# Performance work log

Hardware: AMD Instinct MI355X
Metric: run time of the kernel (lower is better)

The kernel has to match this reference:

```python
import jax, jax.numpy as jnp
import numpy as np
from jax import lax

IMG_H = IMG_W = 800.0
PRE_NMS = 2000      # rpn_pre_nms_top_n (test)
POST_NMS = 1000     # rpn_post_nms_top_n (test)
IOU_THR = 0.7       # rpn nms_thresh
MIN_SIZE = 1e-3     # filter_proposals min_size
SCORE_THR = 0.0     # rpn score_thresh
BBOX_CLIP = float(np.log(1000.0 / 16.0))  # torchvision BoxCoder bbox_xform_clip


def setup_inputs() -> dict:
    key = jax.random.key(0)
    k1, k2, k3, k4 = jax.random.split(key, 4)
    N, A = 8, 1_000_000
    objectness = jax.random.normal(k1, (N, A), jnp.float32)
    deltas = jax.random.normal(k2, (N, A, 4), jnp.float32) * 0.5
    # realistic anchors: random centers inside the image, sizes in [16, 256]
    cxy = jax.random.uniform(k3, (A, 2), jnp.float32) * jnp.array([IMG_W, IMG_H], jnp.float32)
    wh = 16.0 + jax.random.uniform(k4, (A, 2), jnp.float32) * 240.0
    anchors = jnp.concatenate([cxy - 0.5 * wh, cxy + 0.5 * wh], axis=-1)
    return {"objectness": objectness, "deltas": deltas, "anchors": anchors}


def decode_boxes(deltas, anchors):
    # torchvision BoxCoder.decode_single with weights (1,1,1,1)
    wa = anchors[:, 2] - anchors[:, 0]          # [A]
    ha = anchors[:, 3] - anchors[:, 1]
    cxa = anchors[:, 0] + 0.5 * wa
    cya = anchors[:, 1] + 0.5 * ha
    dx, dy = deltas[..., 0], deltas[..., 1]      # [N, A]
    dw = jnp.minimum(deltas[..., 2], BBOX_CLIP)
    dh = jnp.minimum(deltas[..., 3], BBOX_CLIP)
    pcx = dx * wa + cxa
    pcy = dy * ha + cya
    pw = jnp.exp(dw) * wa
    ph = jnp.exp(dh) * ha
    return jnp.stack([pcx - 0.5 * pw, pcy - 0.5 * ph,
                      pcx + 0.5 * pw, pcy + 0.5 * ph], axis=-1)  # [N, A, 4]


def nms_keep(boxes, valid):
    # greedy NMS on score-sorted boxes [K,4]; returns boolean keep mask [K]
    K = boxes.shape[0]
    areas = (boxes[:, 2] - boxes[:, 0]) * (boxes[:, 3] - boxes[:, 1])
    idxs = jnp.arange(K)

    def body(i, keep):
        xx1 = jnp.maximum(boxes[i, 0], boxes[:, 0])
        yy1 = jnp.maximum(boxes[i, 1], boxes[:, 1])
        xx2 = jnp.minimum(boxes[i, 2], boxes[:, 2])
        yy2 = jnp.minimum(boxes[i, 3], boxes[:, 3])
        inter = jnp.maximum(xx2 - xx1, 0.0) * jnp.maximum(yy2 - yy1, 0.0)
        iou = inter / (areas[i] + areas - inter + 1e-12)
        sup = (iou > IOU_THR) & (idxs > i) & keep[i]
        return keep & ~sup

    return lax.fori_loop(0, K, body, valid)


def filter_one(obj, boxes):
    # per-image filter_proposals: top-k -> sigmoid -> clip -> small-box removal -> NMS -> top post_nms
    top_logits, idx = lax.top_k(obj, PRE_NMS)        # sorted desc; sigmoid is monotone
    b = boxes[idx]                                    # [K, 4]
    scores = jax.nn.sigmoid(top_logits)
    x1 = jnp.clip(b[:, 0], 0.0, IMG_W)
    y1 = jnp.clip(b[:, 1], 0.0, IMG_H)
    x2 = jnp.clip(b[:, 2], 0.0, IMG_W)
    y2 = jnp.clip(b[:, 3], 0.0, IMG_H)
    bc = jnp.stack([x1, y1, x2, y2], axis=-1)
    valid = ((x2 - x1) >= MIN_SIZE) & ((y2 - y1) >= MIN_SIZE) & (scores > SCORE_THR)
    keep = nms_keep(lax.stop_gradient(bc), valid)     # selection is non-differentiable
    masked = jnp.where(keep, scores, -jnp.inf)
    _, fidx = lax.top_k(lax.stop_gradient(masked), POST_NMS)
    out_boxes = bc[fidx]                              # [POST_NMS, 4]
    out_scores = jnp.where(keep[fidx], scores[fidx], 0.0)
    return out_boxes, out_scores


def reference(objectness, deltas, anchors):
    proposals = decode_boxes(deltas, anchors)                 # [N, A, 4]
    boxes, scores = jax.vmap(filter_one)(objectness, proposals)
    return jnp.concatenate([boxes, scores[:, :, None]], axis=-1)  # [N, POST_NMS, 5]
```

## Files before the change

kernel.cpp:

```cpp
#include <hip/hip_runtime.h>
#include <cstdint>

#define NIMG 8
#define PRE 2000
#define POST 1000
#define NCH 64
#define CH_CAP 256
#define CAND_TOT (NCH*CH_CAP)
#define NSORT 4
#define SEG 2048
#define CAND_MAX (NSORT*SEG)
#define NPB 64
#define PB_CAP 1024
#define PAIR_CAP 12288
#define JT 256
#define IMGW 800.0f
#define BBOX_CLIP_F 4.135166556742356f
#define STATIC_KMIN 0xC0200000u

#define OFF_BCNT  0
#define OFF_BPCNT (OFF_BCNT + NIMG*NCH*4)
#define OFF_CAND  (OFF_BPCNT + NIMG*NPB*4)
#define OFF_SRT   (OFF_CAND + NIMG*CAND_TOT*8)
#define OFF_BOX   (OFF_SRT + NIMG*CAND_MAX*8)
#define OFF_SCORE (OFF_BOX + NIMG*PRE*16)
#define OFF_VALID (OFF_SCORE + NIMG*PRE*4)
#define OFF_PAIRS (OFF_VALID + NIMG*PRE*4)

__device__ __forceinline__ unsigned int fkey(float f) {
    unsigned int b = __float_as_uint(f);
    return (b & 0x80000000u) ? ~b : (b | 0x80000000u);
}
__device__ __forceinline__ float inv_fkey(unsigned int k) {
    unsigned int b = (k & 0x80000000u) ? (k ^ 0x80000000u) : ~k;
    return __uint_as_float(b);
}

__global__ void k_compact(const float* __restrict__ obj,
                          unsigned long long* __restrict__ cand,
                          unsigned int* __restrict__ bcnt, int A) {
    __shared__ unsigned long long loc[CH_CAP];
    __shared__ unsigned int lcnt;
    const int img = blockIdx.y;
    const int b = blockIdx.x;
    const int t = threadIdx.x;
    if (t == 0) lcnt = 0u;
    __syncthreads();
    const float4* p4 = (const float4*)(obj + (size_t)img * A);
    const int nvec = A >> 2;
    for (int i = b * 256 + t; i < nvec; i += NCH * 256) {
        float4 v = p4[i];
        unsigned int k0 = fkey(v.x), k1 = fkey(v.y), k2 = fkey(v.z), k3 = fkey(v.w);
        unsigned int base = (unsigned int)(i << 2);
        if (k0 >= STATIC_KMIN) { unsigned int p = atomicAdd(&lcnt, 1u); if (p < CH_CAP) loc[p] = ((unsigned long long)k0 << 32) | (0xFFFFFFFFu - base); }
        if (k1 >= STATIC_KMIN) { unsigned int p = atomicAdd(&lcnt, 1u); if (p < CH_CAP) loc[p] = ((unsigned long long)k1 << 32) | (0xFFFFFFFFu - (base + 1u)); }
        if (k2 >= STATIC_KMIN) { unsigned int p = atomicAdd(&lcnt, 1u); if (p < CH_CAP) loc[p] = ((unsigned long long)k2 << 32) | (0xFFFFFFFFu - (base + 2u)); }
        if (k3 >= STATIC_KMIN) { unsigned int p = atomicAdd(&lcnt, 1u); if (p < CH_CAP) loc[p] = ((unsigned long long)k3 << 32) | (0xFFFFFFFFu - (base + 3u)); }
    }
    if (b == 0) {
        const float* p = obj + (size_t)img * A;
        for (int i = (nvec << 2) + t; i < A; i += 256) {
            unsigned int k = fkey(p[i]);
            if (k >= STATIC_KMIN) { unsigned int q = atomicAdd(&lcnt, 1u); if (q < CH_CAP) loc[q] = ((unsigned long long)k << 32) | (0xFFFFFFFFu - (unsigned int)i); }
        }
    }
    __syncthreads();
    if (t == 0) bcnt[img * NCH + b] = lcnt;
    unsigned int n = min(lcnt, (unsigned int)CH_CAP);
    unsigned long long* dst = cand + (size_t)img * CAND_TOT + (size_t)b * CH_CAP;
    for (unsigned int i = t; i < n; i += 256) dst[i] = loc[i];
}

__global__ __launch_bounds__(1024) void k_fallback(const float* __restrict__ obj,
                                                   unsigned long long* __restrict__ cand,
                                                   unsigned int* __restrict__ bcnt, int A) {
    __shared__ unsigned int h[4096];
    __shared__ unsigned int cnts[NCH];
    __shared__ int need_s;
    __shared__ unsigned int kth_s, c2;
    const int img = blockIdx.x;
    const int t = threadIdx.x;
    if (t < NCH) cnts[t] = bcnt[img * NCH + t];
    __syncthreads();
    if (t == 0) {
        unsigned int tot = 0; int bad = 0;
        for (int c = 0; c < NCH; ++c) { unsigned int r = cnts[c]; if (r > CH_CAP) bad = 1; tot += min(r, (unsigned int)CH_CAP); }
        for (int g = 0; g < NSORT; ++g) {
            unsigned int s = 0;
            for (int c = 0; c < NCH / NSORT; ++c) s += min(cnts[g * (NCH / NSORT) + c], (unsigned int)CH_CAP);
            if (s > SEG) bad = 1;
        }
        if (tot < PRE) bad = 1;
        need_s = bad;
    }
    __syncthreads();
    if (!need_s) return;
    for (int i = t; i < 4096; i += 1024) h[i] = 0u;
    __syncthreads();
    const float* p = obj + (size_t)img * A;
    for (int i = t; i < A; i += 1024) atomicAdd(&h[fkey(p[i]) >> 20], 1u);
    __syncthreads();
    if (t == 0) {
        unsigned int run = 0, kb = 0;
        for (int b = 4095; b >= 0; --b) { run += h[b]; if (run >= (unsigned int)PRE) { kb = (unsigned int)b; break; } }
        kth_s = kb << 20; c2 = 0u;
    }
    __syncthreads();
    for (int i = t; i < A; i += 1024) {
        unsigned int k = fkey(p[i]);
        if (k >= kth_s) {
            unsigned int q = atomicAdd(&c2, 1u);
            if (q < CAND_MAX)
                cand[(size_t)img * CAND_TOT + (size_t)(q & (NCH - 1)) * CH_CAP + (q >> 6)] =
                    ((unsigned long long)k << 32) | (0xFFFFFFFFu - (unsigned int)i);
        }
    }
    __syncthreads();
    unsigned int tot = min(c2, (unsigned int)CAND_MAX);
    if (t < NCH) bcnt[img * NCH + t] = (tot + (NCH - 1) - t) >> 6;
}

__global__ __launch_bounds__(1024) void k_sort(const unsigned long long* __restrict__ cand,
                                               const unsigned int* __restrict__ bcnt,
                                               unsigned long long* __restrict__ srt) {
    __shared__ unsigned long long sb[SEG];
    __shared__ unsigned int pref[17];
    const int img = blockIdx.y;
    const int s = blockIdx.x;
    const int t = threadIdx.x;
    if (t == 0) {
        unsigned int o = 0; pref[0] = 0;
        for (int c = 0; c < 16; ++c) {
            unsigned int n = min(bcnt[img * NCH + s * 16 + c], (unsigned int)CH_CAP);
            o += n; if (o > (unsigned int)SEG) o = SEG;
            pref[c + 1] = o;
        }
    }
    for (int i = t; i < SEG; i += 1024) sb[i] = 0ull;
    __syncthreads();
    for (int c = 0; c < 16; ++c) {
        unsigned int b0 = pref[c], n = pref[c + 1] - pref[c];
        const unsigned long long* src = cand + (size_t)img * CAND_TOT + (size_t)(s * 16 + c) * CH_CAP;
        for (unsigned int i = t; i < n; i += 1024) sb[b0 + i] = src[i];
    }
    __syncthreads();
    for (int k = 2; k <= SEG; k <<= 1) {
        for (int j = k >> 1; j > 0; j >>= 1) {
            for (int i = t; i < SEG; i += 1024) {
                int l = i ^ j;
                if (l > i) {
                    unsigned long long a = sb[i], b = sb[l];
                    bool sw = ((i & k) == 0) ? (a < b) : (a > b);
                    if (sw) { sb[i] = b; sb[l] = a; }
                }
            }
            __syncthreads();
        }
    }
    unsigned long long* dst = srt + (size_t)img * CAND_MAX + (size_t)s * SEG;
    for (int i = t; i < SEG; i += 1024) dst[i] = sb[i];
}

__global__ __launch_bounds__(1024) void k_merge_decode(
    const float* __restrict__ deltas, const float* __restrict__ anchors,
    const unsigned long long* __restrict__ srt,
    float* __restrict__ boxes, float* __restrict__ scores, unsigned int* __restrict__ valid, int A) {
    __shared__ unsigned long long sb[CAND_MAX];
    const int img = blockIdx.y;
    const int myseg = blockIdx.x;
    const int t = threadIdx.x;
    const unsigned long long* c = srt + (size_t)img * CAND_MAX;
    for (int i = t; i < CAND_MAX; i += 1024) sb[i] = c[i];
    __syncthreads();
    for (int e2 = t; e2 < SEG; e2 += 1024) {
        const int e = (myseg << 11) + e2;
        unsigned long long v = sb[e];
        if (v == 0ull) continue;
        int rank = e2;
#pragma unroll
        for (int s = 0; s < 4; ++s) {
            if (s == myseg) continue;
            int lo = 0, hi = SEG;
            const unsigned long long* seg = sb + (s << 11);
            while (lo < hi) {
                int mid = (lo + hi) >> 1;
                if (seg[mid] > v) lo = mid + 1; else hi = mid;
            }
            rank += lo;
        }
        if (rank >= PRE) continue;
        unsigned int idx = 0xFFFFFFFFu - (unsigned int)(v & 0xFFFFFFFFull);
        float logit = inv_fkey((unsigned int)(v >> 32));
        float4 d = ((const float4*)deltas)[(size_t)img * A + idx];
        float4 a = ((const float4*)anchors)[idx];
        float wa = a.z - a.x, ha = a.w - a.y;
        float cxa = a.x + 0.5f * wa, cya = a.y + 0.5f * ha;
        float dw = fminf(d.z, BBOX_CLIP_F), dh = fminf(d.w, BBOX_CLIP_F);
        float pcx = d.x * wa + cxa, pcy = d.y * ha + cya;
        float pw = expf(dw) * wa, ph = expf(dh) * ha;
        float x1 = fminf(fmaxf(pcx - 0.5f * pw, 0.0f), IMGW);
        float y1 = fminf(fmaxf(pcy - 0.5f * ph, 0.0f), IMGW);
        float x2 = fminf(fmaxf(pcx + 0.5f * pw, 0.0f), IMGW);
        float y2 = fminf(fmaxf(pcy + 0.5f * ph, 0.0f), IMGW);
        float sc = 1.0f / (1.0f + expf(-logit));
        unsigned int vd = (((x2 - x1) >= 1e-3f) && ((y2 - y1) >= 1e-3f) && (sc > 0.0f)) ? 1u : 0u;
        ((float4*)boxes)[(size_t)img * PRE + rank] = make_float4(x1, y1, x2, y2);
        scores[img * PRE + rank] = sc;
        valid[img * PRE + rank] = vd;
    }
}

__global__ void k_pairs(const float* __restrict__ boxes, unsigned int* __restrict__ pairs,
                        unsigned int* __restrict__ bpcnt) {
#pragma clang fp contract(off)
    const int img = blockIdx.y;
    const int bid = blockIdx.x;
    const int it = bid >> 3;
    const int jc = bid & 7;
    const int t = threadIdx.x;
    if (jc < it) { if (t == 0) bpcnt[img * NPB + bid] = 0u; return; }
    __shared__ float4 jb[JT];
    __shared__ float jar[JT];
    __shared__ unsigned int lp[PB_CAP];
    __shared__ unsigned int lcnt;
    if (t == 0) lcnt = 0u;
    const float4* B = (const float4*)(boxes + (size_t)img * PRE * 4);
    const int j0 = jc * JT;
    const int jn = min(JT, PRE - j0);
    if (t < jn) {
        float4 b = B[j0 + t];
        jb[t] = b;
        jar[t] = (b.z - b.x) * (b.w - b.y);
    }
    const int i = it * JT + t;
    const bool row_ok = (i < PRE);
    float x1 = 0, y1 = 0, x2 = 0, y2 = 0, ai = 0;
    if (row_ok) {
        float4 b = B[i];
        x1 = b.x; y1 = b.y; x2 = b.z; y2 = b.w;
        ai = (b.z - b.x) * (b.w - b.y);
    }
    __syncthreads();
    if (row_ok) {
#pragma unroll 4
        for (int jj = 0; jj < jn; ++jj) {
            float4 bj = jb[jj];
            float aj = jar[jj];
            float xx1 = fmaxf(x1, bj.x);
            float yy1 = fmaxf(y1, bj.y);
            float xx2 = fminf(x2, bj.z);
            float yy2 = fminf(y2, bj.w);
            float iw = fmaxf(xx2 - xx1, 0.0f);
            float ih = fmaxf(yy2 - yy1, 0.0f);
            float inter = iw * ih;
            float iou = inter / (ai + aj - inter + 1e-12f);
            int j = j0 + jj;
            if (iou > 0.7f && j > i) {
                unsigned int p = atomicAdd(&lcnt, 1u);
                if (p < PB_CAP) lp[p] = ((unsigned int)i << 11) | (unsigned int)j;
            }
        }
    }
    __syncthreads();
    unsigned int n = min(lcnt, (unsigned int)PB_CAP);
    if (t == 0) bpcnt[img * NPB + bid] = n;
    unsigned int* dst = pairs + ((size_t)img * NPB + bid) * PB_CAP;
    for (unsigned int q = t; q < n; q += blockDim.x) dst[q] = lp[q];
}

__global__ __launch_bounds__(1024) void k_final(
    const float* __restrict__ boxes, const float* __restrict__ scores, const unsigned int* __restrict__ valid,
    const unsigned int* __restrict__ pairs, const unsigned int* __restrict__ bpcnt, float* __restrict__ out) {
    __shared__ unsigned int pb[PAIR_CAP];
    __shared__ unsigned int bp[NPB];
    __shared__ unsigned int ofs[NPB + 1];
    __shared__ unsigned char vld[2048];
    __shared__ unsigned char alive[2048];
    __shared__ unsigned char kill[2048];
    __shared__ unsigned int incl[2048];
    __shared__ int changed;
    const int img = blockIdx.x;
    const int t = threadIdx.x;
    if (t < NPB) bp[t] = min(bpcnt[img * NPB + t], (unsigned int)PB_CAP);
    __syncthreads();
    if (t == 0) {
        unsigned int o = 0; ofs[0] = 0;
        for (int c = 0; c < NPB; ++c) { o += bp[c]; if (o > (unsigned int)PAIR_CAP) o = PAIR_CAP; ofs[c + 1] = o; }
    }
    for (int i = t; i < 2048; i += 1024) {
        unsigned char v = (i < PRE) ? (unsigned char)valid[img * PRE + i] : 0;
        vld[i] = v;
        alive[i] = v;
    }
    __syncthreads();
    for (int c = 0; c < NPB; ++c) {
        unsigned int b0 = ofs[c], n = ofs[c + 1] - ofs[c];
        const unsigned int* src = pairs + ((size_t)img * NPB + c) * PB_CAP;
        for (unsigned int i = t; i < n; i += 1024) pb[b0 + i] = src[i];
    }
    const int np = (int)ofs[NPB];
    __syncthreads();
    for (int iter = 0; iter < 2048; ++iter) {
        if (t == 0) changed = 0;
        for (int i = t; i < 2048; i += 1024) kill[i] = 0;
        __syncthreads();
        for (int e = t; e < np; e += 1024) {
            unsigned int u = pb[e];
            unsigned int i = u >> 11, j = u & 2047u;
            if (alive[i]) kill[j] = 1;
        }
        __syncthreads();
        for (int i = t; i < 2048; i += 1024) {
            unsigned char na = (vld[i] && !kill[i]) ? 1 : 0;
            if (na != alive[i]) { alive[i] = na; changed = 1; }
        }
        __syncthreads();
        bool done = (changed == 0);
        __syncthreads();
        if (done) break;
    }
    const int i0 = t, i1 = t + 1024;
    incl[i0] = alive[i0]; incl[i1] = alive[i1];
    __syncthreads();
    for (int d = 1; d < 2048; d <<= 1) {
        unsigned int v0 = (i0 >= d) ? incl[i0 - d] : 0u;
        unsigned int v1 = (i1 >= d) ? incl[i1 - d] : 0u;
        __syncthreads();
        incl[i0] += v0; incl[i1] += v1;
        __syncthreads();
    }
    const unsigned int Nk = incl[2047];
    for (int i = t; i < PRE; i += 1024) {
        int slot = -1;
        float sc = 0.0f;
        if (alive[i]) {
            unsigned int r = incl[i] - 1u;
            if (r < (unsigned int)POST) { slot = (int)r; sc = scores[img * PRE + i]; }
        } else if (Nk < (unsigned int)POST) {
            unsigned int rnk = (unsigned int)i - incl[i];
            unsigned int s2 = Nk + rnk;
            if (s2 < (unsigned int)POST) { slot = (int)s2; sc = 0.0f; }
        }
        if (slot >= 0) {
            float4 b = ((const float4*)boxes)[(size_t)img * PRE + i];
            float* o = out + ((size_t)img * POST + slot) * 5;
            o[0] = b.x; o[1] = b.y; o[2] = b.z; o[3] = b.w; o[4] = sc;
        }
    }
}

extern "C" void kernel_launch(void* const* d_in, const int* in_sizes, int n_in,
                              void* d_out, int out_size, void* d_ws, size_t ws_size,
                              hipStream_t stream) {
    const float* obj = (const float*)d_in[0];
    const float* deltas = (const float*)d_in[1];
    const float* anchors = (const float*)d_in[2];
    float* out = (float*)d_out;
    const int A = in_sizes[0] / NIMG;

    char* ws = (char*)d_ws;
    unsigned int* bcnt = (unsigned int*)(ws + OFF_BCNT);
    unsigned int* bpcnt = (unsigned int*)(ws + OFF_BPCNT);
    unsigned long long* cand = (unsigned long long*)(ws + OFF_CAND);
    unsigned long long* srt = (unsigned long long*)(ws + OFF_SRT);
    float* boxes = (float*)(ws + OFF_BOX);
    float* scores = (float*)(ws + OFF_SCORE);
    unsigned int* valid = (unsigned int*)(ws + OFF_VALID);
    unsigned int* pairs = (unsigned int*)(ws + OFF_PAIRS);

    k_compact<<<dim3(NCH, NIMG), dim3(256), 0, stream>>>(obj, cand, bcnt, A);
    k_fallback<<<dim3(NIMG), dim3(1024), 0, stream>>>(obj, cand, bcnt, A);
    k_sort<<<dim3(NSORT, NIMG), dim3(1024), 0, stream>>>(cand, bcnt, srt);
    k_merge_decode<<<dim3(NSORT, NIMG), dim3(1024), 0, stream>>>(deltas, anchors, srt, boxes, scores, valid, A);
    k_pairs<<<dim3(NPB, NIMG), dim3(256), 0, stream>>>(boxes, pairs, bpcnt);
    k_final<<<dim3(NIMG), dim3(1024), 0, stream>>>(boxes, scores, valid, pairs, bpcnt, out);
}
```

Measured before the change: 300.4 us.

## Fuse fallback, segment sort and merge-decode into one kernel with inter-block barrier

Merges the fallback, bitonic segment sort and merge/decode kernels into a single kernel. The four segment blocks of each image synchronise through a global atomic counter spin barrier before ranking across segments. The fallback path now runs inside each block, with every block redoing the histogram and keeping a strided subset of candidates. Compaction also doubles the chunk count and halves the per-chunk capacity. The aim is to cut two kernel launches and their gaps, at the cost of relying on all blocks being co-resident and of redundant fallback work when the fallback fires.

```diff
diff --git a/kernel.cpp b/kernel.cpp
--- a/kernel.cpp
+++ b/kernel.cpp
@@ -4,10 +4,11 @@
 #define NIMG 8
 #define PRE 2000
 #define POST 1000
-#define NCH 64
-#define CH_CAP 256
+#define NCH 128
+#define CH_CAP 128
 #define CAND_TOT (NCH*CH_CAP)
 #define NSORT 4
+#define GPS (NCH/NSORT)
 #define SEG 2048
 #define CAND_MAX (NSORT*SEG)
 #define NPB 64
@@ -19,11 +20,12 @@
 #define STATIC_KMIN 0xC0200000u
 
 #define OFF_BCNT  0
-#define OFF_BPCNT (OFF_BCNT + NIMG*NCH*4)
+#define OFF_DONE  (OFF_BCNT + NIMG*NCH*4)
+#define OFF_BPCNT (OFF_DONE + 1024)
 #define OFF_CAND  (OFF_BPCNT + NIMG*NPB*4)
-#define OFF_SRT   (OFF_CAND + NIMG*CAND_TOT*8)
-#define OFF_BOX   (OFF_SRT + NIMG*CAND_MAX*8)
-#define OFF_SCORE (OFF_BOX + NIMG*PRE*16)
+#define OFF_SRT   (OFF_CAND + (size_t)NIMG*CAND_TOT*8)
+#define OFF_BOX   (OFF_SRT + (size_t)NIMG*CAND_MAX*8)
+#define OFF_SCORE (OFF_BOX + (size_t)NIMG*PRE*16)
 #define OFF_VALID (OFF_SCORE + NIMG*PRE*4)
 #define OFF_PAIRS (OFF_VALID + NIMG*PRE*4)
 
@@ -38,13 +40,17 @@
 
 __global__ void k_compact(const float* __restrict__ obj,
                           unsigned long long* __restrict__ cand,
-                          unsigned int* __restrict__ bcnt, int A) {
+                          unsigned int* __restrict__ bcnt,
+                          unsigned int* __restrict__ done, int A) {
     __shared__ unsigned long long loc[CH_CAP];
     __shared__ unsigned int lcnt;
     const int img = blockIdx.y;
     const int b = blockIdx.x;
     const int t = threadIdx.x;
-    if (t == 0) lcnt = 0u;
+    if (t == 0) {
+        lcnt = 0u;
+        if (b == 0) done[img * 32] = 0u;
+    }
     __syncthreads();
     const float4* p4 = (const float4*)(obj + (size_t)img * A);
     const int nvec = A >> 2;
@@ -71,79 +77,74 @@
     for (unsigned int i = t; i < n; i += 256) dst[i] = loc[i];
 }
 
-__global__ __launch_bounds__(1024) void k_fallback(const float* __restrict__ obj,
-                                                   unsigned long long* __restrict__ cand,
-                                                   unsigned int* __restrict__ bcnt, int A) {
-    __shared__ unsigned int h[4096];
+__global__ __launch_bounds__(1024) void k_sortmerge(
+    const float* __restrict__ obj, const float* __restrict__ deltas, const float* __restrict__ anchors,
+    unsigned long long* __restrict__ cand, const unsigned int* __restrict__ bcnt,
+    unsigned long long* __restrict__ srt, unsigned int* __restrict__ done,
+    float* __restrict__ boxes, float* __restrict__ scores, unsigned int* __restrict__ valid, int A) {
+    __shared__ unsigned long long sb[3 * SEG];
     __shared__ unsigned int cnts[NCH];
-    __shared__ int need_s;
-    __shared__ unsigned int kth_s, c2;
-    const int img = blockIdx.x;
+    __shared__ unsigned int pref[GPS + 1];
+    __shared__ unsigned int kth_s, lcnt;
+    __shared__ int bad_s;
+    const int img = blockIdx.y;
+    const int myseg = blockIdx.x;
     const int t = threadIdx.x;
+
     if (t < NCH) cnts[t] = bcnt[img * NCH + t];
     __syncthreads();
     if (t == 0) {
-        unsigned int tot = 0; int bad = 0;
+        int bad = 0; unsigned int tot = 0;
         for (int c = 0; c < NCH; ++c) { unsigned int r = cnts[c]; if (r > CH_CAP) bad = 1; tot += min(r, (unsigned int)CH_CAP); }
         for (int g = 0; g < NSORT; ++g) {
             unsigned int s = 0;
-            for (int c = 0; c < NCH / NSORT; ++c) s += min(cnts[g * (NCH / NSORT) + c], (unsigned int)CH_CAP);
-            if (s > SEG) bad = 1;
-        }
-        if (tot < PRE) bad = 1;
-        need_s = bad;
-    }
-    __syncthreads();
-    if (!need_s) return;
-    for (int i = t; i < 4096; i += 1024) h[i] = 0u;
-    __syncthreads();
-    const float* p = obj + (size_t)img * A;
-    for (int i = t; i < A; i += 1024) atomicAdd(&h[fkey(p[i]) >> 20], 1u);
-    __syncthreads();
-    if (t == 0) {
-        unsigned int run = 0, kb = 0;
-        for (int b = 4095; b >= 0; --b) { run += h[b]; if (run >= (unsigned int)PRE) { kb = (unsigned int)b; break; } }
-        kth_s = kb << 20; c2 = 0u;
-    }
-    __syncthreads();
-    for (int i = t; i < A; i += 1024) {
-        unsigned int k = fkey(p[i]);
-        if (k >= kth_s) {
-            unsigned int q = atomicAdd(&c2, 1u);
-            if (q < CAND_MAX)
-                cand[(size_t)img * CAND_TOT + (size_t)(q & (NCH - 1)) * CH_CAP + (q >> 6)] =
-                    ((unsigned long long)k << 32) | (0xFFFFFFFFu - (unsigned int)i);
-        }
-    }
-    __syncthreads();
-    unsigned int tot = min(c2, (unsigned int)CAND_MAX);
-    if (t < NCH) bcnt[img * NCH + t] = (tot + (NCH - 1) - t) >> 6;
-}
-
-__global__ __launch_bounds__(1024) void k_sort(const unsigned long long* __restrict__ cand,
-                                               const unsigned int* __restrict__ bcnt,
-                                               unsigned long long* __restrict__ srt) {
-    __shared__ unsigned long long sb[SEG];
-    __shared__ unsigned int pref[17];
-    const int img = blockIdx.y;
-    const int s = blockIdx.x;
-    const int t = threadIdx.x;
-    if (t == 0) {
-        unsigned int o = 0; pref[0] = 0;
-        for (int c = 0; c < 16; ++c) {
-            unsigned int n = min(bcnt[img * NCH + s * 16 + c], (unsigned int)CH_CAP);
-            o += n; if (o > (unsigned int)SEG) o = SEG;
-            pref[c + 1] = o;
-        }
-    }
+            for (int c = 0; c < GPS; ++c) s += min(cnts[g * GPS + c], (unsigned int)CH_CAP);
+            if (s > (unsigned int)SEG) bad = 1;
+        }
+        if (tot < (unsigned int)PRE) bad = 1;
+        bad_s = bad;
+        if (!bad) {
+            unsigned int o = 0; pref[0] = 0;
+            for (int c = 0; c < GPS; ++c) { o += min(cnts[myseg * GPS + c], (unsigned int)CH_CAP); pref[c + 1] = o; }
+        }
+    }
+    __syncthreads();
+
     for (int i = t; i < SEG; i += 1024) sb[i] = 0ull;
     __syncthreads();
-    for (int c = 0; c < 16; ++c) {
-        unsigned int b0 = pref[c], n = pref[c + 1] - pref[c];
-        const unsigned long long* src = cand + (size_t)img * CAND_TOT + (size_t)(s * 16 + c) * CH_CAP;
-        for (unsigned int i = t; i < n; i += 1024) sb[b0 + i] = src[i];
-    }
-    __syncthreads();
+
+    if (!bad_s) {
+        const int c = t >> 5, lane = t & 31;
+        const unsigned int b0 = pref[c], n = pref[c + 1] - pref[c];
+        const unsigned long long* src = cand + (size_t)img * CAND_TOT + (size_t)(myseg * GPS + c) * CH_CAP;
+        for (unsigned int i = lane; i < n; i += 32) sb[b0 + i] = src[i];
+    } else {
+        unsigned int* h = (unsigned int*)sb;
+        for (int i = t; i < 4096; i += 1024) h[i] = 0u;
+        __syncthreads();
+        const float* p = obj + (size_t)img * A;
+        for (int i = t; i < A; i += 1024) atomicAdd(&h[fkey(p[i]) >> 20], 1u);
+        __syncthreads();
+        if (t == 0) {
+            unsigned int run = 0, kb = 0;
+            for (int b = 4095; b >= 0; --b) { run += h[b]; if (run >= (unsigned int)PRE) { kb = (unsigned int)b; break; } }
+            kth_s = kb << 20;
+        }
+        __syncthreads();
+        for (int i = t; i < SEG; i += 1024) sb[i] = 0ull;
+        if (t == 0) lcnt = 0u;
+        __syncthreads();
+        for (int i = t; i < A; i += 1024) {
+            unsigned int k = fkey(p[i]);
+            if (k >= kth_s && (i & (NSORT - 1)) == myseg) {
+                unsigned int q = atomicAdd(&lcnt, 1u);
+                if (q < (unsigned int)SEG)
+                    sb[q] = ((unsigned long long)k << 32) | (0xFFFFFFFFu - (unsigned int)i);
+            }
+        }
+    }
+    __syncthreads();
+
     for (int k = 2; k <= SEG; k <<= 1) {
         for (int j = k >> 1; j > 0; j >>= 1) {
             for (int i = t; i < SEG; i += 1024) {
@@ -157,31 +158,40 @@
             __syncthreads();
         }
     }
-    unsigned long long* dst = srt + (size_t)img * CAND_MAX + (size_t)s * SEG;
-    for (int i = t; i < SEG; i += 1024) dst[i] = sb[i];
-}
-
-__global__ __launch_bounds__(1024) void k_merge_decode(
-    const float* __restrict__ deltas, const float* __restrict__ anchors,
-    const unsigned long long* __restrict__ srt,
-    float* __restrict__ boxes, float* __restrict__ scores, unsigned int* __restrict__ valid, int A) {
-    __shared__ unsigned long long sb[CAND_MAX];
-    const int img = blockIdx.y;
-    const int myseg = blockIdx.x;
-    const int t = threadIdx.x;
-    const unsigned long long* c = srt + (size_t)img * CAND_MAX;
-    for (int i = t; i < CAND_MAX; i += 1024) sb[i] = c[i];
-    __syncthreads();
+
+    unsigned long long* seg_out = srt + (size_t)img * CAND_MAX + (size_t)myseg * SEG;
+    for (int i = t; i < SEG; i += 1024) seg_out[i] = sb[i];
+    __syncthreads();
+    unsigned int* dn = done + img * 32;
+    if (t == 0) {
+        __threadfence();
+        atomicAdd(dn, 1u);
+        while (atomicAdd(dn, 0u) < (unsigned int)NSORT) __builtin_amdgcn_s_sleep(8);
+    }
+    __syncthreads();
+    __threadfence();
+
+    const unsigned long long* simg = srt + (size_t)img * CAND_MAX;
+    {
+        int q = 0;
+        for (int s2 = 0; s2 < NSORT; ++s2) {
+            if (s2 == myseg) continue;
+            const unsigned long long* src = simg + (size_t)s2 * SEG;
+            for (int i = t; i < SEG; i += 1024) sb[q * SEG + i] = src[i];
+            ++q;
+        }
+    }
+    __syncthreads();
+
+    const unsigned long long* own = simg + (size_t)myseg * SEG;
     for (int e2 = t; e2 < SEG; e2 += 1024) {
-        const int e = (myseg << 11) + e2;
-        unsigned long long v = sb[e];
+        unsigned long long v = own[e2];
         if (v == 0ull) continue;
         int rank = e2;
 #pragma unroll
-        for (int s = 0; s < 4; ++s) {
-            if (s == myseg) continue;
+        for (int q = 0; q < NSORT - 1; ++q) {
             int lo = 0, hi = SEG;
-            const unsigned long long* seg = sb + (s << 11);
+            const unsigned long long* seg = sb + q * SEG;
             while (lo < hi) {
                 int mid = (lo + hi) >> 1;
                 if (seg[mid] > v) lo = mid + 1; else hi = mid;
@@ -360,6 +370,7 @@
 
     char* ws = (char*)d_ws;
     unsigned int* bcnt = (unsigned int*)(ws + OFF_BCNT);
+    unsigned int* done = (unsigned int*)(ws + OFF_DONE);
     unsigned int* bpcnt = (unsigned int*)(ws + OFF_BPCNT);
     unsigned long long* cand = (unsigned long long*)(ws + OFF_CAND);
     unsigned long long* srt = (unsigned long long*)(ws + OFF_SRT);
@@ -368,10 +379,8 @@
     unsigned int* valid = (unsigned int*)(ws + OFF_VALID);
     unsigned int* pairs = (unsigned int*)(ws + OFF_PAIRS);
 
-    k_compact<<<dim3(NCH, NIMG), dim3(256), 0, stream>>>(obj, cand, bcnt, A);
-    k_fallback<<<dim3(NIMG), dim3(1024), 0, stream>>>(obj, cand, bcnt, A);
-    k_sort<<<dim3(NSORT, NIMG), dim3(1024), 0, stream>>>(cand, bcnt, srt);
-    k_merge_decode<<<dim3(NSORT, NIMG), dim3(1024), 0, stream>>>(deltas, anchors, srt, boxes, scores, valid, A);
+    k_compact<<<dim3(NCH, NIMG), dim3(256), 0, stream>>>(obj, cand, bcnt, done, A);
+    k_sortmerge<<<dim3(NSORT, NIMG), dim3(1024), 0, stream>>>(obj, deltas, anchors, cand, bcnt, srt, done, boxes, scores, valid, A);
     k_pairs<<<dim3(NPB, NIMG), dim3(256), 0, stream>>>(boxes, pairs, bpcnt);
     k_final<<<dim3(NIMG), dim3(1024), 0, stream>>>(boxes, scores, valid, pairs, bpcnt, out);
 }
```

Result: no change. 304.7 us (+1.4%).
